# Kernel optimization log

Measured on AMD Instinct MI355X. Metric: run time of the kernel, lower is better.

Reference implementation:

```python
import jax, jax.numpy as jnp
import numpy as np

NUM_CLASSES = 21
IOU_THRESH = 0.5
NEG_POS_RATIO = 3
VAR0, VAR1 = 0.1, 0.2


def point_form(priors):
    # (cx,cy,w,h) -> (xmin,ymin,xmax,ymax)
    return jnp.concatenate([priors[:, :2] - priors[:, 2:] / 2,
                            priors[:, :2] + priors[:, 2:] / 2], axis=-1)


def jaccard(box_a, box_b):
    # box_a: [n,4] point form, box_b: [N,4] point form -> [n,N]
    max_xy = jnp.minimum(box_a[:, None, 2:], box_b[None, :, 2:])
    min_xy = jnp.maximum(box_a[:, None, :2], box_b[None, :, :2])
    inter = jnp.prod(jnp.clip(max_xy - min_xy, 0.0, None), axis=-1)
    area_a = jnp.prod(box_a[:, 2:] - box_a[:, :2], axis=-1)[:, None]
    area_b = jnp.prod(box_b[:, 2:] - box_b[:, :2], axis=-1)[None, :]
    return inter / (area_a + area_b - inter)


def encode(matched, priors):
    # matched: [N,4] point form, priors: [N,4] center form
    g_cxcy = ((matched[:, :2] + matched[:, 2:]) / 2 - priors[:, :2]) / (VAR0 * priors[:, 2:])
    g_wh = jnp.log((matched[:, 2:] - matched[:, :2]) / priors[:, 2:]) / VAR1
    return jnp.concatenate([g_cxcy, g_wh], axis=-1)


def match_one(truths, labels, priors):
    # truths: [n_obj,4], labels: [n_obj], priors: [N,4] center form
    ov = jaccard(truths, point_form(priors))          # [n_obj, N]
    best_prior_idx = jnp.argmax(ov, axis=1)           # [n_obj]
    best_truth_overlap = jnp.max(ov, axis=0)          # [N]
    best_truth_idx = jnp.argmax(ov, axis=0)           # [N]
    best_truth_overlap = best_truth_overlap.at[best_prior_idx].set(2.0)
    def body(j, bti):
        return bti.at[best_prior_idx[j]].set(j)
    best_truth_idx = jax.lax.fori_loop(0, truths.shape[0], body, best_truth_idx)
    matched = truths[best_truth_idx]                  # [N,4]
    conf = labels[best_truth_idx].astype(jnp.int32) + 1
    conf = jnp.where(best_truth_overlap < IOU_THRESH, 0, conf)
    return encode(matched, priors), conf


def smooth_l1(x):
    ax = jnp.abs(x)
    return jnp.where(ax < 1.0, 0.5 * x * x, ax - 0.5)


def setup_inputs() -> dict:
    key = jax.random.key(0)
    k1, k2, k3, k4, k5, k6, k7 = jax.random.split(key, 7)
    B, N, n_obj = 128, 8732, 16
    loc_data = jax.random.normal(k1, (B, N, 4), jnp.float32)
    conf_data = jax.random.normal(k2, (B, N, NUM_CLASSES), jnp.float32)
    # valid ground-truth boxes in [0,1], point form, plus class label in [0,20)
    mins = jax.random.uniform(k3, (B, n_obj, 2)) * 0.6
    sizes = jax.random.uniform(k4, (B, n_obj, 2)) * 0.35 + 0.05
    labels = jax.random.randint(k5, (B, n_obj), 0, NUM_CLASSES - 1).astype(jnp.float32)
    targets = jnp.concatenate([mins, mins + sizes, labels[..., None]], axis=-1)
    # priors in center form with positive w,h
    centers = jax.random.uniform(k6, (N, 2))
    wh = jax.random.uniform(k7, (N, 2)) * 0.5 + 0.05
    priors = jnp.concatenate([centers, wh], axis=-1).astype(jnp.float32)
    return {"loc_data": loc_data, "conf_data": conf_data, "targets": targets, "priors": priors}


def _forward(loc_data, conf_data, targets, priors):
    B, N = loc_data.shape[0], loc_data.shape[1]
    truths, labels = targets[:, :, :4], targets[:, :, 4]
    target_loc, target_conf = jax.vmap(match_one, in_axes=(0, 0, None))(truths, labels, priors)
    pos = target_conf > 0                             # [B,N]
    # localization: smooth-L1 summed over positive priors
    loss_l = jnp.sum(smooth_l1(loc_data - target_loc) * pos[..., None].astype(loc_data.dtype))
    # per-prior CE surrogate: logsumexp - logit[target]
    lse = jax.nn.logsumexp(conf_data, axis=-1)        # [B,N]
    gathered = jnp.take_along_axis(conf_data, target_conf[..., None], axis=-1)[..., 0]
    loss_c_all = lse - gathered                       # [B,N]
    # hard negative mining via double argsort ranking (positives excluded)
    lc = jnp.where(pos, 0.0, loss_c_all)
    loss_idx = jnp.argsort(-lc, axis=1)
    idx_rank = jnp.argsort(loss_idx, axis=1)
    num_pos = jnp.sum(pos.astype(jnp.int32), axis=1, keepdims=True)   # [B,1]
    num_neg = jnp.minimum(NEG_POS_RATIO * num_pos, N - 1)
    neg = idx_rank < num_neg
    sel = pos | neg
    loss_c = jnp.sum(jnp.where(sel, loss_c_all, 0.0))
    n_total = jnp.sum(num_pos).astype(loc_data.dtype)
    return loss_l / n_total, loss_c / n_total


def reference(loc_data, conf_data, targets, priors):
    return _forward(loc_data, conf_data, targets, priors)
```

## Files before the change

### kernel.cpp

```cpp
#include <hip/hip_runtime.h>
#include <cstdint>
#include <cstddef>

#define HB1 4096
#define HB2 2048
#define CMAX 21
#define IOU_T 0.5f

__device__ __forceinline__ float sl1(float x) {
    float ax = fabsf(x);
    return ax < 1.0f ? 0.5f * x * x : ax - 0.5f;
}

__global__ __launch_bounds__(256) void kA_best_prior(
    const float* __restrict__ targets, const float* __restrict__ priors,
    float* __restrict__ bpi_val, int* __restrict__ bpi_idx,
    int* __restrict__ num_pos_g, float* __restrict__ accB_g,
    float* __restrict__ acc_g, unsigned* __restrict__ done_g,
    int N, int NOBJ, int SLICES, int CHUNK, int B)
{
    const int s = blockIdx.x, b = blockIdx.y, t = threadIdx.x;
    __shared__ float tb[16 * 4];
    __shared__ float ta[16];
    __shared__ float wv[4 * 16];
    __shared__ int   wi[4 * 16];

    if (s == 0 && b == 0) {
        for (int q = t; q < B; q += 256) num_pos_g[q] = 0;
        for (int q = t; q < 2 * B; q += 256) accB_g[q] = 0.f;
        if (t < 4) acc_g[t] = 0.f;
        if (t == 0) *done_g = 0u;
    }

    if (t < 16) {
        if (t < NOBJ) {
            const float* tr = targets + ((size_t)b * NOBJ + t) * 5;
            float x0 = tr[0], y0 = tr[1], x1 = tr[2], y1 = tr[3];
            tb[t * 4 + 0] = x0; tb[t * 4 + 1] = y0;
            tb[t * 4 + 2] = x1; tb[t * 4 + 3] = y1;
            ta[t] = (x1 - x0) * (y1 - y0);
        } else {
            tb[t * 4 + 0] = 0.f; tb[t * 4 + 1] = 0.f;
            tb[t * 4 + 2] = 0.f; tb[t * 4 + 3] = 0.f;
            ta[t] = 0.f;
        }
    }
    __syncthreads();

    float bv[16]; int bi[16];
#pragma unroll
    for (int j = 0; j < 16; j++) { bv[j] = -1.0f; bi[j] = 0x7fffffff; }

    const int start = s * CHUNK;
    const int end = min(start + CHUNK, N);
    for (int i = start + t; i < end; i += 256) {
        float4 p = ((const float4*)priors)[i];
        float bx0 = p.x - p.z * 0.5f, by0 = p.y - p.w * 0.5f;
        float bx1 = p.x + p.z * 0.5f, by1 = p.y + p.w * 0.5f;
        float ab = (bx1 - bx0) * (by1 - by0);
#pragma unroll
        for (int j = 0; j < 16; j++) {
            float iw = fminf(tb[j * 4 + 2], bx1) - fmaxf(tb[j * 4 + 0], bx0);
            float ih = fminf(tb[j * 4 + 3], by1) - fmaxf(tb[j * 4 + 1], by0);
            iw = fmaxf(iw, 0.f); ih = fmaxf(ih, 0.f);
            float inter = iw * ih;
            float iou = inter / (ta[j] + ab - inter);
            if (iou > bv[j] || (iou == bv[j] && i < bi[j])) { bv[j] = iou; bi[j] = i; }
        }
    }

#pragma unroll
    for (int off = 32; off >= 1; off >>= 1) {
#pragma unroll
        for (int j = 0; j < 16; j++) {
            float v2 = __shfl_down(bv[j], off, 64);
            int   i2 = __shfl_down(bi[j], off, 64);
            if (v2 > bv[j] || (v2 == bv[j] && i2 < bi[j])) { bv[j] = v2; bi[j] = i2; }
        }
    }
    const int wid = t >> 6, lane = t & 63;
    if (lane == 0) {
#pragma unroll
        for (int j = 0; j < 16; j++) { wv[wid * 16 + j] = bv[j]; wi[wid * 16 + j] = bi[j]; }
    }
    __syncthreads();
    if (t < 16) {
        float v = wv[t]; int idx = wi[t];
#pragma unroll
        for (int w = 1; w < 4; w++) {
            float v2 = wv[w * 16 + t]; int i2 = wi[w * 16 + t];
            if (v2 > v || (v2 == v && i2 < idx)) { v = v2; idx = i2; }
        }
        if (t < NOBJ) {
            int o = (b * SLICES + s) * 16 + t;
            bpi_val[o] = v;
            bpi_idx[o] = idx;
        }
    }
}

#define IOU_STEP(j) { \
    float4 tj = tb4[j]; \
    float taj = (tj.z - tj.x) * (tj.w - tj.y); \
    float iw = fminf(tj.z, bx1) - fmaxf(tj.x, bx0); \
    float ih = fminf(tj.w, by1) - fmaxf(tj.y, by0); \
    iw = fmaxf(iw, 0.f); ih = fmaxf(ih, 0.f); \
    float inter = iw * ih; \
    float iou = inter * __builtin_amdgcn_rcpf(taj + ab - inter); \
    if (iou > bto) { bto = iou; bti = (j); } }

__global__ __launch_bounds__(256, 3) void kB_main(
    const float* __restrict__ loc, const float* __restrict__ conf,
    const float* __restrict__ targets, const float* __restrict__ priors,
    const float* __restrict__ bpi_val, const int* __restrict__ bpi_idx,
    float* __restrict__ lc_out, int* __restrict__ num_pos, float* __restrict__ accB,
    int N, int NOBJ, int SLICES, int TPB, int BPB)
{
    const int g = blockIdx.x;
    const int b = g / BPB;
    const int j0 = g % BPB;
    const int t = threadIdx.x;
    const int wid = t >> 6, lane = t & 63;

    __shared__ __align__(16) float buf[2][256 * CMAX];
    __shared__ __align__(16) float tb[16 * 4];
    __shared__ float tl[16];
    __shared__ __align__(16) int bpi_s[16];
    __shared__ float wred[4 * 3];

    if (t < 16) {
        if (t < NOBJ) {
            const float* tr = targets + ((size_t)b * NOBJ + t) * 5;
            tb[t * 4 + 0] = tr[0]; tb[t * 4 + 1] = tr[1];
            tb[t * 4 + 2] = tr[2]; tb[t * 4 + 3] = tr[3];
            tl[t] = tr[4];
            float bv = -1.f; int bi = 0x7fffffff;
            for (int s2 = 0; s2 < SLICES; s2++) {
                int o = (b * SLICES + s2) * 16 + t;
                float v = bpi_val[o]; int idx = bpi_idx[o];
                if (v > bv || (v == bv && idx < bi)) { bv = v; bi = idx; }
            }
            bpi_s[t] = bi;
        } else {
            tb[t * 4 + 0] = 0.f; tb[t * 4 + 1] = 0.f; tb[t * 4 + 2] = 0.f; tb[t * 4 + 3] = 0.f;
            tl[t] = 0.f; bpi_s[t] = -1;
        }
    }

    const float* confB = conf + (size_t)b * N * CMAX;
    const float* locB  = loc + (size_t)b * N * 4;

    float4 r0, r1, r2, r3, r4, r5, pld, ppr;

    auto stage = [&](int xx) {
        int i0s = xx * 256;
        int rows_s = min(256, N - i0s);
        int nf4s = (rows_s * CMAX) >> 2;
        const float4* s4 = (const float4*)(confB + (size_t)i0s * CMAX);
        if (t + 0    < nf4s) r0 = s4[t + 0];
        if (t + 256  < nf4s) r1 = s4[t + 256];
        if (t + 512  < nf4s) r2 = s4[t + 512];
        if (t + 768  < nf4s) r3 = s4[t + 768];
        if (t + 1024 < nf4s) r4 = s4[t + 1024];
        if (t + 1280 < nf4s) r5 = s4[t + 1280];
        if (t < rows_s) {
            ppr = ((const float4*)priors)[i0s + t];
            pld = ((const float4*)locB)[i0s + t];
        }
    };

    float ll = 0.f, plc = 0.f, np = 0.f;
    int x = j0, p = 0;
    if (x < TPB) stage(x);

    while (x < TPB) {
        const int i0 = x * 256;
        const int rows = min(256, N - i0);
        const int nf4 = (rows * CMAX) >> 2;

        float4 myp = ppr, myl = pld;

        float4* bp4f = (float4*)buf[p];
        if (t + 0    < nf4) bp4f[t + 0]    = r0;
        if (t + 256  < nf4) bp4f[t + 256]  = r1;
        if (t + 512  < nf4) bp4f[t + 512]  = r2;
        if (t + 768  < nf4) bp4f[t + 768]  = r3;
        if (t + 1024 < nf4) bp4f[t + 1024] = r4;
        if (t + 1280 < nf4) bp4f[t + 1280] = r5;
        __syncthreads();

        int xn = x + BPB;
        if (xn < TPB) stage(xn);

        if (t < rows) {
            const int i = i0 + t;
            float4 pp = myp;
            float bx0 = pp.x - pp.z * 0.5f, by0 = pp.y - pp.w * 0.5f;
            float bx1 = pp.x + pp.z * 0.5f, by1 = pp.y + pp.w * 0.5f;
            float ab = (bx1 - bx0) * (by1 - by0);
            float bto = -1.f; int bti = 0;
            const float4* tb4 = (const float4*)tb;
            if (NOBJ == 16) {
#pragma unroll
                for (int j = 0; j < 16; j++) IOU_STEP(j);
            } else {
                for (int j = 0; j < NOBJ; j++) IOU_STEP(j);
            }
            const int4* bp4 = (const int4*)bpi_s;
#pragma unroll
            for (int jj = 0; jj < 4; jj++) {
                int4 q = bp4[jj];
                if (q.x == i) { bto = 2.0f; bti = jj * 4 + 0; }
                if (q.y == i) { bto = 2.0f; bti = jj * 4 + 1; }
                if (q.z == i) { bto = 2.0f; bti = jj * 4 + 2; }
                if (q.w == i) { bto = 2.0f; bti = jj * 4 + 3; }
            }
            bool pos = !(bto < IOU_T);
            if (pos) {
                float4 tj = tb4[bti];
                float rz = __builtin_amdgcn_rcpf(pp.z);
                float rw = __builtin_amdgcn_rcpf(pp.w);
                float gcx = ((tj.x + tj.z) * 0.5f - pp.x) * (10.0f * rz);
                float gcy = ((tj.y + tj.w) * 0.5f - pp.y) * (10.0f * rw);
                float gw = __logf((tj.z - tj.x) * rz) * 5.0f;
                float gh = __logf((tj.w - tj.y) * rw) * 5.0f;
                ll += sl1(myl.x - gcx) + sl1(myl.y - gcy) + sl1(myl.z - gw) + sl1(myl.w - gh);
                np += 1.f;
            }
            int cf = pos ? ((int)tl[bti] + 1) : 0;
            const float* cr = buf[p] + t * CMAX;
            float m = cr[0];
#pragma unroll
            for (int c = 1; c < CMAX; c++) m = fmaxf(m, cr[c]);
            float ssum = 0.f;
#pragma unroll
            for (int c = 0; c < CMAX; c++) ssum += __expf(cr[c] - m);
            float lse = m + __logf(ssum);
            float lossc = lse - cr[cf];
            if (pos) plc += lossc;
            float lcv = pos ? 0.f : lossc;
            lcv = fmaxf(lcv, 0.f);
            lc_out[(size_t)b * N + i] = lcv;
        }
        p ^= 1;
        x = xn;
    }

#pragma unroll
    for (int off = 32; off >= 1; off >>= 1) {
        ll  += __shfl_down(ll, off, 64);
        plc += __shfl_down(plc, off, 64);
        np  += __shfl_down(np, off, 64);
    }
    if (lane == 0) { wred[wid * 3 + 0] = ll; wred[wid * 3 + 1] = plc; wred[wid * 3 + 2] = np; }
    __syncthreads();
    if (t == 0) {
        float a0 = 0.f, a1 = 0.f, a2 = 0.f;
#pragma unroll
        for (int w = 0; w < 4; w++) { a0 += wred[w * 3 + 0]; a1 += wred[w * 3 + 1]; a2 += wred[w * 3 + 2]; }
        atomicAdd(&accB[b * 2 + 0], a0);
        atomicAdd(&accB[b * 2 + 1], a1);
        atomicAdd(&num_pos[b], (int)a2);
    }
}

__device__ __forceinline__ void wave_sufscan(int& c, float& s, int lane) {
#pragma unroll
    for (int off = 1; off < 64; off <<= 1) {
        int c2 = __shfl_down(c, off, 64);
        float s2 = __shfl_down(s, off, 64);
        if (lane + off < 64) { c += c2; s += s2; }
    }
}

__global__ __launch_bounds__(1024) void kC_topk(
    const float* __restrict__ lc, const int* __restrict__ num_pos,
    const float* __restrict__ accB,
    float* __restrict__ acc, unsigned* __restrict__ done_ctr,
    float* __restrict__ out, int N, int B)
{
    const int b = blockIdx.x, t = threadIdx.x;
    const int NT = 1024;
    const int wid = t >> 6, lane = t & 63;
    __shared__ __align__(16) int   cnt[HB1];
    __shared__ __align__(16) float sm[HB1];
    __shared__ int   wc[16];
    __shared__ float ws[16];
    __shared__ int s_strad, s_krem;
    __shared__ float s_above;
    __shared__ int s_last;
    __shared__ float wsum[16], wsA[16], wsB[16];

    const int k = min(3 * num_pos[b], N - 1);
    const float* lcb = lc + (size_t)b * N;
    float total = 0.f;

    if (k > 0) {
        ((int4*)cnt)[t] = make_int4(0, 0, 0, 0);
        ((float4*)sm)[t] = make_float4(0.f, 0.f, 0.f, 0.f);
        __syncthreads();
        const int n4 = N >> 2;
        const float4* lcb4 = (const float4*)lcb;
        for (int i = t; i < n4; i += NT) {
            float4 v = lcb4[i];
            { unsigned u = __float_as_uint(v.x) >> 19; atomicAdd(&cnt[u], 1); atomicAdd(&sm[u], v.x); }
            { unsigned u = __float_as_uint(v.y) >> 19; atomicAdd(&cnt[u], 1); atomicAdd(&sm[u], v.y); }
            { unsigned u = __float_as_uint(v.z) >> 19; atomicAdd(&cnt[u], 1); atomicAdd(&sm[u], v.z); }
            { unsigned u = __float_as_uint(v.w) >> 19; atomicAdd(&cnt[u], 1); atomicAdd(&sm[u], v.w); }
        }
        for (int i = (n4 << 2) + t; i < N; i += NT) {
            float v = lcb[i];
            unsigned u = __float_as_uint(v) >> 19;
            atomicAdd(&cnt[u], 1); atomicAdd(&sm[u], v);
        }
        __syncthreads();
        {
            int4  cv = ((const int4*)cnt)[t];
            float4 sv = ((const float4*)sm)[t];
            int   ci = cv.x + cv.y + cv.z + cv.w;
            float si = sv.x + sv.y + sv.z + sv.w;
            wave_sufscan(ci, si, lane);
            if (lane == 0) { wc[wid] = ci; ws[wid] = si; }
            __syncthreads();
            int cab = 0; float sab = 0.f;
            for (int w = wid + 1; w < 16; w++) { cab += wc[w]; sab += ws[w]; }
            int   i0c = ci + cab;          float f0 = si + sab;
            int   i1c = i0c - cv.x;        float f1 = f0 - sv.x;
            int   i2c = i1c - cv.y;        float f2 = f1 - sv.y;
            int   i3c = i2c - cv.z;        float f3 = f2 - sv.z;
            int   i4c = i3c - cv.w;
            if (i1c < k && k <= i0c) { s_strad = 4 * t + 0; s_krem = k - i1c; s_above = f1; }
            if (i2c < k && k <= i1c) { s_strad = 4 * t + 1; s_krem = k - i2c; s_above = f2; }
            if (i3c < k && k <= i2c) { s_strad = 4 * t + 2; s_krem = k - i3c; s_above = f3; }
            if (i4c < k && k <= i3c) { s_strad = 4 * t + 3; s_krem = k - i4c; s_above = f3 - sv.w; }
        }
        __syncthreads();
        const int s1 = s_strad, k2 = s_krem;
        total += s_above;

        __syncthreads();
        ((int2*)cnt)[t] = make_int2(0, 0);
        ((float2*)sm)[t] = make_float2(0.f, 0.f);
        __syncthreads();
        for (int i = t; i < N; i += NT) {
            float v = lcb[i];
            unsigned u = __float_as_uint(v);
            if ((int)(u >> 19) == s1) {
                int q = (int)((u >> 8) & 0x7FF);
                atomicAdd(&cnt[q], 1); atomicAdd(&sm[q], v);
            }
        }
        __syncthreads();
        {
            int2  cv = ((const int2*)cnt)[t];
            float2 sv = ((const float2*)sm)[t];
            int   ci = cv.x + cv.y;
            float si = sv.x + sv.y;
            wave_sufscan(ci, si, lane);
            if (lane == 0) { wc[wid] = ci; ws[wid] = si; }
            __syncthreads();
            int cab = 0; float sab = 0.f;
            for (int w = wid + 1; w < 16; w++) { cab += wc[w]; sab += ws[w]; }
            int   i0c = ci + cab;       float f0 = si + sab;
            int   i1c = i0c - cv.x;     float f1 = f0 - sv.x;
            int   i2c = i1c - cv.y;
            if (i1c < k2 && k2 <= i0c) { s_strad = 2 * t + 0; s_krem = k2 - i1c; s_above = f1; }
            if (i2c < k2 && k2 <= i1c) { s_strad = 2 * t + 1; s_krem = k2 - i2c; s_above = f1 - sv.y; }
        }
        __syncthreads();
        const int s2 = s_strad, krem = s_krem;
        total += s_above;
        float tval = __uint_as_float((((unsigned)s1) << 19) | (((unsigned)s2) << 8));
        total += (float)krem * tval;
    }

    if (t == 0) {
        if (k > 0) atomicAdd(&acc[1], total);
        __threadfence();
        unsigned old = atomicAdd(done_ctr, 1u);
        s_last = (old == (unsigned)gridDim.x - 1u) ? 1 : 0;
    }
    __syncthreads();
    if (s_last) {
        __threadfence();
        float vn = 0.f, va = 0.f, vb = 0.f;
        for (int q = t; q < B; q += NT) {
            vn += (float)num_pos[q];
            va += accB[q * 2 + 0];
            vb += accB[q * 2 + 1];
        }
#pragma unroll
        for (int off = 32; off >= 1; off >>= 1) {
            vn += __shfl_down(vn, off, 64);
            va += __shfl_down(va, off, 64);
            vb += __shfl_down(vb, off, 64);
        }
        if (lane == 0) { wsum[wid] = vn; wsA[wid] = va; wsB[wid] = vb; }
        __syncthreads();
        if (t == 0) {
            float n = 0.f, a = 0.f, bsum = 0.f;
#pragma unroll
            for (int w = 0; w < 16; w++) { n += wsum[w]; a += wsA[w]; bsum += wsB[w]; }
            float l2 = atomicAdd(&acc[1], 0.0f);
            out[0] = a / n;
            out[1] = (bsum + l2) / n;
        }
    }
}

extern "C" void kernel_launch(void* const* d_in, const int* in_sizes, int n_in,
                              void* d_out, int out_size, void* d_ws, size_t ws_size,
                              hipStream_t stream)
{
    const float* loc     = (const float*)d_in[0];
    const float* conf    = (const float*)d_in[1];
    const float* targets = (const float*)d_in[2];
    const float* priors  = (const float*)d_in[3];
    float* out = (float*)d_out;

    const int N = in_sizes[3] / 4;
    const int BN = in_sizes[0] / 4;
    const int B = BN / N;
    const int NOBJ = in_sizes[2] / (B * 5);
    const int SLICES = 8;
    const int CHUNK = (N + SLICES - 1) / SLICES;
    const int TPB = (N + 255) / 256;
    const int BPB = 6;

    char* w = (char*)d_ws;
    float*    lc_ws   = (float*)w;                         size_t off = (size_t)BN * 4;
    float*    bpi_val = (float*)(w + off);                 off += (size_t)B * SLICES * 16 * 4;
    int*      bpi_idx = (int*)(w + off);                   off += (size_t)B * SLICES * 16 * 4;
    int*      num_pos = (int*)(w + off);                   off += (size_t)B * 4;
    float*    accB    = (float*)(w + off);                 off += (size_t)B * 2 * 4;
    float*    acc     = (float*)(w + off);                 off += 16;
    unsigned* done    = (unsigned*)(w + off);              off += 16;

    dim3 gA(SLICES, B);
    kA_best_prior<<<gA, 256, 0, stream>>>(targets, priors, bpi_val, bpi_idx,
                                          num_pos, accB, acc, done, N, NOBJ, SLICES, CHUNK, B);

    kB_main<<<B * BPB, 256, 0, stream>>>(loc, conf, targets, priors, bpi_val, bpi_idx,
                                         lc_ws, num_pos, accB, N, NOBJ, SLICES, TPB, BPB);

    kC_topk<<<B, 1024, 0, stream>>>(lc_ws, num_pos, accB, acc, done, out, N, B);
}
```

Before: 225.7 us.

## Give each wave a private LDS tile to drop block barriers in kB_main

Each of the four waves now owns its own 64-row slice of the conf tile in shared memory, so staging into LDS and reading back no longer need a block-wide __syncthreads per tile or double buffering. The per-block LDS footprint falls to one tile, launch bounds are raised to 6 blocks per CU, and the grid grows from 6 to 8 blocks per batch. A scalar tail copy handles rows whose float count is not a multiple of four. The wave-private LDS write then read relies on in-wave ordering, which leaves less room to overlap global loads with compute inside a wave.

```diff
diff --git a/kernel.cpp b/kernel.cpp
--- a/kernel.cpp
+++ b/kernel.cpp
@@ -109,7 +109,7 @@
     float iou = inter * __builtin_amdgcn_rcpf(taj + ab - inter); \
     if (iou > bto) { bto = iou; bti = (j); } }
 
-__global__ __launch_bounds__(256, 3) void kB_main(
+__global__ __launch_bounds__(256, 6) void kB_main(
     const float* __restrict__ loc, const float* __restrict__ conf,
     const float* __restrict__ targets, const float* __restrict__ priors,
     const float* __restrict__ bpi_val, const int* __restrict__ bpi_idx,
@@ -122,7 +122,7 @@
     const int t = threadIdx.x;
     const int wid = t >> 6, lane = t & 63;
 
-    __shared__ __align__(16) float buf[2][256 * CMAX];
+    __shared__ __align__(16) float buf[4][64 * CMAX];
     __shared__ __align__(16) float tb[16 * 4];
     __shared__ float tl[16];
     __shared__ __align__(16) int bpi_s[16];
@@ -146,54 +146,62 @@
             tl[t] = 0.f; bpi_s[t] = -1;
         }
     }
+    __syncthreads();
 
     const float* confB = conf + (size_t)b * N * CMAX;
     const float* locB  = loc + (size_t)b * N * 4;
-
-    float4 r0, r1, r2, r3, r4, r5, pld, ppr;
+    float* myLDS = buf[wid];
+
+    float4 r0 = {}, r1 = {}, r2 = {}, r3 = {}, r4 = {}, r5 = {};
+    float4 pld = {}, ppr = {};
 
     auto stage = [&](int xx) {
-        int i0s = xx * 256;
-        int rows_s = min(256, N - i0s);
+        int row0 = xx * 256 + wid * 64;
+        if (row0 >= N) return;
+        int rows_s = min(64, N - row0);
         int nf4s = (rows_s * CMAX) >> 2;
-        const float4* s4 = (const float4*)(confB + (size_t)i0s * CMAX);
-        if (t + 0    < nf4s) r0 = s4[t + 0];
-        if (t + 256  < nf4s) r1 = s4[t + 256];
-        if (t + 512  < nf4s) r2 = s4[t + 512];
-        if (t + 768  < nf4s) r3 = s4[t + 768];
-        if (t + 1024 < nf4s) r4 = s4[t + 1024];
-        if (t + 1280 < nf4s) r5 = s4[t + 1280];
-        if (t < rows_s) {
-            ppr = ((const float4*)priors)[i0s + t];
-            pld = ((const float4*)locB)[i0s + t];
+        const float4* s4 = (const float4*)(confB + (size_t)row0 * CMAX);
+        if (lane + 0   < nf4s) r0 = s4[lane + 0];
+        if (lane + 64  < nf4s) r1 = s4[lane + 64];
+        if (lane + 128 < nf4s) r2 = s4[lane + 128];
+        if (lane + 192 < nf4s) r3 = s4[lane + 192];
+        if (lane + 256 < nf4s) r4 = s4[lane + 256];
+        if (lane + 320 < nf4s) r5 = s4[lane + 320];
+        if (lane < rows_s) {
+            ppr = ((const float4*)priors)[row0 + lane];
+            pld = ((const float4*)locB)[row0 + lane];
         }
     };
 
     float ll = 0.f, plc = 0.f, np = 0.f;
-    int x = j0, p = 0;
-    if (x < TPB) stage(x);
+    int x = j0;
+    stage(x);
 
     while (x < TPB) {
-        const int i0 = x * 256;
-        const int rows = min(256, N - i0);
+        const int row0 = x * 256 + wid * 64;
+        const int rows = (row0 < N) ? min(64, N - row0) : 0;
         const int nf4 = (rows * CMAX) >> 2;
 
         float4 myp = ppr, myl = pld;
 
-        float4* bp4f = (float4*)buf[p];
-        if (t + 0    < nf4) bp4f[t + 0]    = r0;
-        if (t + 256  < nf4) bp4f[t + 256]  = r1;
-        if (t + 512  < nf4) bp4f[t + 512]  = r2;
-        if (t + 768  < nf4) bp4f[t + 768]  = r3;
-        if (t + 1024 < nf4) bp4f[t + 1024] = r4;
-        if (t + 1280 < nf4) bp4f[t + 1280] = r5;
-        __syncthreads();
+        float4* d4 = (float4*)myLDS;
+        if (lane + 0   < nf4) d4[lane + 0]   = r0;
+        if (lane + 64  < nf4) d4[lane + 64]  = r1;
+        if (lane + 128 < nf4) d4[lane + 128] = r2;
+        if (lane + 192 < nf4) d4[lane + 192] = r3;
+        if (lane + 256 < nf4) d4[lane + 256] = r4;
+        if (lane + 320 < nf4) d4[lane + 320] = r5;
+        {
+            int nf = rows * CMAX;
+            int rem = nf - (nf4 << 2);
+            if (lane < rem) myLDS[(nf4 << 2) + lane] = confB[(size_t)row0 * CMAX + (nf4 << 2) + lane];
+        }
 
         int xn = x + BPB;
         if (xn < TPB) stage(xn);
 
-        if (t < rows) {
-            const int i = i0 + t;
+        if (lane < rows) {
+            const int i = row0 + lane;
             float4 pp = myp;
             float bx0 = pp.x - pp.z * 0.5f, by0 = pp.y - pp.w * 0.5f;
             float bx1 = pp.x + pp.z * 0.5f, by1 = pp.y + pp.w * 0.5f;
@@ -228,7 +236,7 @@
                 np += 1.f;
             }
             int cf = pos ? ((int)tl[bti] + 1) : 0;
-            const float* cr = buf[p] + t * CMAX;
+            const float* cr = myLDS + lane * CMAX;
             float m = cr[0];
 #pragma unroll
             for (int c = 1; c < CMAX; c++) m = fmaxf(m, cr[c]);
@@ -242,7 +250,6 @@
             lcv = fmaxf(lcv, 0.f);
             lc_out[(size_t)b * N + i] = lcv;
         }
-        p ^= 1;
         x = xn;
     }
 
@@ -425,7 +432,7 @@
     const int SLICES = 8;
     const int CHUNK = (N + SLICES - 1) / SLICES;
     const int TPB = (N + 255) / 256;
-    const int BPB = 6;
+    const int BPB = 8;
 
     char* w = (char*)d_ws;
     float*    lc_ws   = (float*)w;                         size_t off = (size_t)BN * 4;
```

Measured after the change: 322.9 us. +43.0%, slower.
